# Kernel tuning notes

Measured on AMD Instinct MI355X. Metric: run time of the kernel, lower is better.

## Reference

```python
import jax, jax.numpy as jnp
import numpy as np

NEG_INF = -9e15  # matches torch's -9000000000000000.0 mask value
ALPHA = 0.2      # LeakyReLU negative slope


def setup_inputs() -> dict:
    key = jax.random.key(0)
    k1, k2, k3, k4 = jax.random.split(key, 4)
    B, N, Fin, Fout = 8, 2048, 256, 256
    h = jax.random.normal(k1, (B, N, Fin), dtype=jnp.float32)
    adj = jax.random.randint(k2, (B, N, N), 0, 2, dtype=jnp.int32)
    # xavier_uniform with gain=1.414
    limW = 1.414 * np.sqrt(6.0 / (Fin + Fout))
    W = jax.random.uniform(k3, (Fin, Fout), minval=-limW, maxval=limW, dtype=jnp.float32)
    lima = 1.414 * np.sqrt(6.0 / (2 * Fout + 1))
    a = jax.random.uniform(k4, (2 * Fout, 1), minval=-lima, maxval=lima, dtype=jnp.float32)
    return {"h": h, "adj": adj, "W": W, "a": a}


def reference(h, adj, W, a):
    # h: (B, N, Fin), adj: (B, N, N), W: (Fin, Fout), a: (2*Fout, 1)
    Fout = W.shape[1]
    Wh = jnp.einsum('bni,io->bno', h, W)                 # (B, N, Fout)
    # e[b,i,j] = leakyrelu(Wh[b,i] @ a1 + Wh[b,j] @ a2) -- equivalent to the
    # original concat([Wh_i, Wh_j]) @ a without the O(N^2 * 2F) intermediate.
    e1 = Wh @ a[:Fout, 0]                                # (B, N)
    e2 = Wh @ a[Fout:, 0]                                # (B, N)
    e = jax.nn.leaky_relu(e1[:, :, None] + e2[:, None, :], negative_slope=ALPHA)
    masked = jnp.where(adj > 0, e, NEG_INF)
    attention = jax.nn.softmax(masked, axis=-1)          # (B, N, N)
    # dropout omitted (deterministic eval-mode reference)
    h_prime = jnp.einsum('bij,bjo->bio', attention, Wh)  # (B, N, Fout)
    return jax.nn.elu(h_prime), attention
```

## Files before the change

kernel.cpp:

```cpp
#include <hip/hip_runtime.h>
#include <hip/hip_bf16.h>
#include <stdint.h>

#define NEG_INF -9.0e15f
#define LRELU_ALPHA 0.2f
#define LOG2E 1.442695040888963f

using bf16x8  = __attribute__((ext_vector_type(8))) short;
using f32x4   = __attribute__((ext_vector_type(4))) float;
using short4v = __attribute__((ext_vector_type(4))) short;
using int4v   = __attribute__((ext_vector_type(4))) int;
using float4v = __attribute__((ext_vector_type(4))) float;
using uint2v  = __attribute__((ext_vector_type(2))) unsigned;
using uint4v  = __attribute__((ext_vector_type(4))) unsigned;

static __device__ __forceinline__ short f2bf(float f) {
  unsigned u = __builtin_bit_cast(unsigned, f);
  u = u + 0x7FFFu + ((u >> 16) & 1u);
  return (short)(u >> 16);
}
static __device__ __forceinline__ unsigned cvtpk_bf16(float lo, float hi) {
  unsigned r;
  asm volatile("v_cvt_pk_bf16_f32 %0, %1, %2" : "=v"(r) : "v"(lo), "v"(hi));
  return r;
}
static __device__ __forceinline__ void gload16(const void* g, void* l) {
  __builtin_amdgcn_global_load_lds((const __attribute__((address_space(1))) void*)g,
                                   (__attribute__((address_space(3))) void*)l, 16, 0, 0);
}

__global__ __launch_bounds__(256) void prep_kernel(
    const float* __restrict__ W, const float* __restrict__ a,
    short* __restrict__ W_t, float* __restrict__ aW1, float* __restrict__ aW2)
{
  const int bid = blockIdx.x;
  const int tid = threadIdx.x;
  if (bid < 16) {
    __shared__ float t[64][65];
    const int m0 = (bid & 3) * 64, n0 = (bid >> 2) * 64;
    const int rr = tid >> 3, cc = (tid & 7) * 8;
#pragma unroll
    for (int p = 0; p < 2; ++p) {
      int row = rr + p * 32;
      const float* sp = W + (m0 + row) * 256 + n0 + cc;
      float4v v0 = *(const float4v*)sp;
      float4v v1 = *(const float4v*)(sp + 4);
#pragma unroll
      for (int j = 0; j < 4; ++j) { t[row][cc + j] = v0[j]; t[row][cc + 4 + j] = v1[j]; }
    }
    __syncthreads();
#pragma unroll
    for (int p = 0; p < 2; ++p) {
      int orow = rr + p * 32;
      short vv[8] __attribute__((aligned(16)));
#pragma unroll
      for (int j = 0; j < 8; ++j) vv[j] = f2bf(t[cc + j][orow]);
      short* dp = W_t + (n0 + orow) * 256 + m0 + cc;
      *(int4v*)dp = *(const int4v*)vv;
    }
  } else {
    const int r8 = tid >> 3, o4 = (tid & 7) * 4;
    float s1[8] = {}, s2[8] = {};
#pragma unroll
    for (int rp = 0; rp < 8; ++rp) {
      int row = r8 + rp * 32;
#pragma unroll
      for (int k = 0; k < 8; ++k) {
        int o = o4 + k * 32;
        float4v wv = *(const float4v*)(W + row * 256 + o);
        float4v a1 = *(const float4v*)(a + o);
        float4v a2 = *(const float4v*)(a + 256 + o);
#pragma unroll
        for (int e = 0; e < 4; ++e) { s1[rp] += wv[e] * a1[e]; s2[rp] += wv[e] * a2[e]; }
      }
    }
#pragma unroll
    for (int rp = 0; rp < 8; ++rp) {
#pragma unroll
      for (int off = 4; off > 0; off >>= 1) {
        s1[rp] += __shfl_xor(s1[rp], off, 64);
        s2[rp] += __shfl_xor(s2[rp], off, 64);
      }
      if ((tid & 7) == 0) { aW1[r8 + rp * 32] = s1[rp]; aW2[r8 + rp * 32] = s2[rp]; }
    }
  }
}

__global__ __launch_bounds__(256) void gemm_h_kernel(
    const float* __restrict__ A, const short* __restrict__ Bt,
    short* __restrict__ Wht, const float* __restrict__ aW1,
    const float* __restrict__ aW2, float* __restrict__ e1, float* __restrict__ e2)
{
  __shared__ short As[128 * 32];
  __shared__ short Bs[128 * 32];
  __shared__ short T[128][136];
  const int m0 = blockIdx.x * 128, n0 = blockIdx.y * 128;
  const int tid = threadIdx.x;
  const int w = tid >> 6, lane = tid & 63;
  const int wr = w >> 1, wc = w & 1;
  const int g = lane >> 4, lr = lane & 15;
  const bool doE = (blockIdx.y == 0);

  f32x4 acc[4][4] = {};
  float s1q[2] = {0.f, 0.f}, s2q[2] = {0.f, 0.f};

  for (int k0 = 0; k0 < 256; k0 += 32) {
    __syncthreads();
#pragma unroll
    for (int q = 0; q < 2; ++q) {
      int c = q * 256 + tid;
      int row = c >> 2, kq = (c & 3) << 3;
      const float* ap = A + (long long)(m0 + row) * 256 + k0 + kq;
      float4v u0 = *(const float4v*)ap;
      float4v u1 = *(const float4v*)(ap + 4);
      if (doE) {
        float4v w1a = *(const float4v*)(aW1 + k0 + kq);
        float4v w1b = *(const float4v*)(aW1 + k0 + kq + 4);
        float4v w2a = *(const float4v*)(aW2 + k0 + kq);
        float4v w2b = *(const float4v*)(aW2 + k0 + kq + 4);
#pragma unroll
        for (int e = 0; e < 4; ++e) {
          s1q[q] += u0[e] * w1a[e] + u1[e] * w1b[e];
          s2q[q] += u0[e] * w2a[e] + u1[e] * w2b[e];
        }
      }
      uint4v uv;
      uv[0] = cvtpk_bf16(u0[0], u0[1]);
      uv[1] = cvtpk_bf16(u0[2], u0[3]);
      uv[2] = cvtpk_bf16(u1[0], u1[1]);
      uv[3] = cvtpk_bf16(u1[2], u1[3]);
      *(bf16x8*)(As + c * 8) = __builtin_bit_cast(bf16x8, uv);
    }
#pragma unroll
    for (int q = 0; q < 2; ++q) {
      int p = w * 2 + q;
      int c = p * 64 + lane;
      int row = c >> 2, kq = (c & 3) << 3;
      gload16(Bt + (long long)(n0 + row) * 256 + k0 + kq, Bs + p * 512);
    }
    __syncthreads();

    bf16x8 af[4], bfr[4];
#pragma unroll
    for (int i = 0; i < 4; ++i) {
      af[i]  = *(const bf16x8*)(As + (wr * 64 + i * 16 + lr) * 32 + 8 * g);
      bfr[i] = *(const bf16x8*)(Bs + (wc * 64 + i * 16 + lr) * 32 + 8 * g);
    }
#pragma unroll
    for (int i = 0; i < 4; ++i)
#pragma unroll
      for (int j = 0; j < 4; ++j)
        acc[i][j] = __builtin_amdgcn_mfma_f32_16x16x32_bf16(af[i], bfr[j], acc[i][j], 0, 0, 0);
  }

  if (doE) {
#pragma unroll
    for (int q = 0; q < 2; ++q) {
      float a1 = s1q[q], a2 = s2q[q];
      a1 += __shfl_xor(a1, 1, 64); a1 += __shfl_xor(a1, 2, 64);
      a2 += __shfl_xor(a2, 1, 64); a2 += __shfl_xor(a2, 2, 64);
      if ((tid & 3) == 0) {
        int row = m0 + q * 64 + (tid >> 2);
        e1[row] = a1; e2[row] = a2;
      }
    }
  }

  __syncthreads();
#pragma unroll
  for (int i = 0; i < 4; ++i) {
    int row_base = wr * 64 + i * 16 + 4 * g;
#pragma unroll
    for (int j = 0; j < 4; ++j) {
      int col = wc * 64 + j * 16 + lr;
#pragma unroll
      for (int r = 0; r < 4; ++r)
        T[col][row_base + r] = f2bf(acc[i][j][r]);
    }
  }
  __syncthreads();
  const int b = m0 >> 11, mloc = m0 & 2047;
  short* wb = Wht + (long long)b * 524288 + mloc;
#pragma unroll
  for (int p = 0; p < 8; ++p) {
    int c = (tid >> 4) + p * 16;
    int off = (tid & 15) * 8;
    bf16x8 v = *(const bf16x8*)(&T[c][off]);
    *(bf16x8*)(wb + (long long)(n0 + c) * 2048 + off) = v;
  }
}

__global__ __launch_bounds__(256) void pack_kernel(
    const int* __restrict__ adj, const float* __restrict__ e1,
    const float* __restrict__ e2, float* __restrict__ attn)
{
  const int i = blockIdx.x;
  const int b = blockIdx.y;
  const long long row = (long long)b * 2048 + i;
  const int tid = threadIdx.x;
  const int wid = tid >> 6, lane = tid & 63;
  const int j0 = tid * 8;

  const int*   arow = adj + row * 2048 + j0;
  const float  ei   = e1[row];
  const float* e2b  = e2 + b * 2048 + j0;

  int4v   a0 = *(const int4v*)(arow);
  int4v   a1 = *(const int4v*)(arow + 4);
  float4v f0 = *(const float4v*)(e2b);
  float4v f1 = *(const float4v*)(e2b + 4);

  float s[8];
#pragma unroll
  for (int k = 0; k < 8; ++k) {
    float x = ei + (k < 4 ? f0[k] : f1[k - 4]);
    float v = fmaxf(x, LRELU_ALPHA * x);
    int  ad = (k < 4 ? a0[k] : a1[k - 4]);
    s[k] = (ad > 0) ? v : NEG_INF;
  }
  float m = s[0];
#pragma unroll
  for (int k = 1; k < 8; ++k) m = fmaxf(m, s[k]);
#pragma unroll
  for (int off = 32; off > 0; off >>= 1) m = fmaxf(m, __shfl_xor(m, off, 64));

  __shared__ float wmax[4], wsum[4];
  if (lane == 0) wmax[wid] = m;
  __syncthreads();
  const float M = fmaxf(fmaxf(wmax[0], wmax[1]), fmaxf(wmax[2], wmax[3]));

  float p[8]; float t = 0.f;
#pragma unroll
  for (int k = 0; k < 8; ++k) { p[k] = __expf(s[k] - M); t += p[k]; }
#pragma unroll
  for (int off = 32; off > 0; off >>= 1) t += __shfl_xor(t, off, 64);
  if (lane == 0) wsum[wid] = t;
  __syncthreads();
  const float S = wsum[0] + wsum[1] + wsum[2] + wsum[3];
  const float r = 1.0f / S;

  uint4v uv;
  uv[0] = cvtpk_bf16(p[0] * r, p[1] * r);
  uv[1] = cvtpk_bf16(p[2] * r, p[3] * r);
  uv[2] = cvtpk_bf16(p[4] * r, p[5] * r);
  uv[3] = cvtpk_bf16(p[6] * r, p[7] * r);
  short* op = (short*)(attn + row * 2048 + 1024) + j0;
  *(uint4v*)op = uv;
}

__global__ __launch_bounds__(256, 4) void pv_kernel(
    const short* __restrict__ Bt, float* __restrict__ attnw, float* __restrict__ C)
{
  __shared__ short As0[32 * 32],  As1[32 * 32];
  __shared__ short Bs0[256 * 32], Bs1[256 * 32];
  const int bid = blockIdx.x;
  const int bz  = bid & 7;
  const int M0  = (bid >> 3) << 5;
  const int tid = threadIdx.x;
  const int w = tid >> 6, lane = tid & 63;
  const int g = lane >> 4, lr = lane & 15;

  Bt    += (long long)bz * 524288;
  attnw += (long long)bz * 4194304;
  C     += (long long)bz * 524288;

  const int pr = tid >> 3, k4 = (tid & 7) << 2;
  const int kc = k4 >> 3;
  const int as_off = pr * 32 + ((kc ^ ((pr >> 1) & 3)) << 3) + (k4 & 7);
  float* arow = attnw + (long long)(M0 + pr) * 2048;

  const int bcol_off = lane >> 2;
  const int bchunk   = (lane & 3) ^ ((lane >> 3) & 3);

  const int a_s  = w * 64 + lane;
  const int a_r  = a_s >> 2, a_cs = a_s & 3;
  const int a_dc = a_cs ^ ((a_r >> 1) & 3);
  const short* aP = (const short*)(attnw + (long long)(M0 + a_r) * 2048 + 1024) + a_dc * 8;

  f32x4 acc[2][4] = {};

  auto STAGE = [&](short* BsD, short* AsD, int k0) {
#pragma unroll
    for (int q = 0; q < 4; ++q) {
      int pp = w * 4 + q;
      int col = pp * 16 + bcol_off;
      gload16(Bt + (long long)col * 2048 + k0 + bchunk * 8, BsD + pp * 512);
    }
    if (w < 2) gload16(aP + k0, AsD + w * 512);
  };

  auto COMPUTE = [&](const short* BsD, const short* AsD, int k0) {
    uint2v pw = *(const uint2v*)(AsD + as_off);
    float4v o;
    o[0] = __builtin_bit_cast(float, pw[0] << 16);
    o[1] = __builtin_bit_cast(float, pw[0] & 0xFFFF0000u);
    o[2] = __builtin_bit_cast(float, pw[1] << 16);
    o[3] = __builtin_bit_cast(float, pw[1] & 0xFFFF0000u);
    *(float4v*)(arow + k0 + k4) = o;

    bf16x8 af[2], bfr[4];
#pragma unroll
    for (int i = 0; i < 2; ++i) {
      int row = i * 16 + lr;
      af[i] = *(const bf16x8*)(AsD + row * 32 + ((g ^ ((row >> 1) & 3)) << 3));
    }
#pragma unroll
    for (int j = 0; j < 4; ++j) {
      int col = w * 64 + j * 16 + lr;
      bfr[j] = *(const bf16x8*)(BsD + col * 32 + ((g ^ ((col >> 1) & 3)) << 3));
    }
#pragma unroll
    for (int i = 0; i < 2; ++i)
#pragma unroll
      for (int j = 0; j < 4; ++j)
        acc[i][j] = __builtin_amdgcn_mfma_f32_16x16x32_bf16(af[i], bfr[j], acc[i][j], 0, 0, 0);
  };

  STAGE(Bs0, As0, 0);
  __syncthreads();
  for (int t = 0; t < 64; t += 2) {
    STAGE(Bs1, As1, (t + 1) * 32);
    COMPUTE(Bs0, As0, t * 32);
    __syncthreads();
    if (t + 2 < 64) STAGE(Bs0, As0, (t + 2) * 32);
    COMPUTE(Bs1, As1, (t + 1) * 32);
    __syncthreads();
  }

#pragma unroll
  for (int i = 0; i < 2; ++i) {
    int row_base = M0 + i * 16 + 4 * g;
#pragma unroll
    for (int j = 0; j < 4; ++j) {
      int col = w * 64 + j * 16 + lr;
#pragma unroll
      for (int r = 0; r < 4; ++r) {
        float v = acc[i][j][r];
        v = (v > 0.f) ? v : (__expf(v) - 1.f);
        C[(long long)(row_base + r) * 256 + col] = v;
      }
    }
  }
}

extern "C" void kernel_launch(void* const* d_in, const int* in_sizes, int n_in,
                              void* d_out, int out_size, void* d_ws, size_t ws_size,
                              hipStream_t stream)
{
  const float* h   = (const float*)d_in[0];
  const int*   adj = (const int*)d_in[1];
  const float* W   = (const float*)d_in[2];
  const float* a   = (const float*)d_in[3];

  float* hp_out   = (float*)d_out;
  float* attn_out = hp_out + 4194304LL;

  short* W_t  = (short*)d_ws;
  short* Wh_t = W_t + 65536;
  float* e1   = (float*)(Wh_t + 4194304);
  float* e2   = e1 + 16384;
  float* aW1  = e2 + 16384;
  float* aW2  = aW1 + 256;

  prep_kernel<<<17, 256, 0, stream>>>(W, a, W_t, aW1, aW2);
  gemm_h_kernel<<<dim3(128, 2), 256, 0, stream>>>(h, W_t, Wh_t, aW1, aW2, e1, e2);
  pack_kernel<<<dim3(2048, 8), 256, 0, stream>>>(adj, e1, e2, attn_out);
  pv_kernel<<<512, 256, 0, stream>>>(Wh_t, attn_out, hp_out);
}
```

Before: 121.9 us.

## Write fp32 attention in softmax kernel and convert to bf16 inside PV

The softmax kernel now writes the final fp32 attention directly, where it used to store a packed bf16 copy in the second half of each output row. The PV kernel stages fp32 attention tiles into LDS with an XOR swizzle and converts them to bf16 just before the MFMA. This removes the per-tile fp32 writeback that PV previously did from its bf16 staging buffer. Total attention traffic is roughly unchanged; the trade is that PV becomes read-only on attention but loads twice the bytes per tile, and its LDS tiles double in size, so launch bounds drop from 4 to 3 blocks. LeakyReLU is also rewritten as a select.

```diff
diff --git a/kernel.cpp b/kernel.cpp
--- a/kernel.cpp
+++ b/kernel.cpp
@@ -190,7 +190,7 @@
   }
 }
 
-__global__ __launch_bounds__(256) void pack_kernel(
+__global__ __launch_bounds__(256) void attn_softmax_kernel(
     const int* __restrict__ adj, const float* __restrict__ e1,
     const float* __restrict__ e2, float* __restrict__ attn)
 {
@@ -214,7 +214,7 @@
 #pragma unroll
   for (int k = 0; k < 8; ++k) {
     float x = ei + (k < 4 ? f0[k] : f1[k - 4]);
-    float v = fmaxf(x, LRELU_ALPHA * x);
+    float v = x > 0.f ? x : LRELU_ALPHA * x;
     int  ad = (k < 4 ? a0[k] : a1[k - 4]);
     s[k] = (ad > 0) ? v : NEG_INF;
   }
@@ -239,19 +239,18 @@
   const float S = wsum[0] + wsum[1] + wsum[2] + wsum[3];
   const float r = 1.0f / S;
 
-  uint4v uv;
-  uv[0] = cvtpk_bf16(p[0] * r, p[1] * r);
-  uv[1] = cvtpk_bf16(p[2] * r, p[3] * r);
-  uv[2] = cvtpk_bf16(p[4] * r, p[5] * r);
-  uv[3] = cvtpk_bf16(p[6] * r, p[7] * r);
-  short* op = (short*)(attn + row * 2048 + 1024) + j0;
-  *(uint4v*)op = uv;
-}
-
-__global__ __launch_bounds__(256, 4) void pv_kernel(
-    const short* __restrict__ Bt, float* __restrict__ attnw, float* __restrict__ C)
-{
-  __shared__ short As0[32 * 32],  As1[32 * 32];
+  float4v o0, o1;
+#pragma unroll
+  for (int k = 0; k < 4; ++k) { o0[k] = p[k] * r; o1[k] = p[k + 4] * r; }
+  float* op = attn + row * 2048 + j0;
+  *(float4v*)op       = o0;
+  *(float4v*)(op + 4) = o1;
+}
+
+__global__ __launch_bounds__(256, 3) void pv_kernel(
+    const float* __restrict__ attn, const short* __restrict__ Bt, float* __restrict__ C)
+{
+  __shared__ float As0[32 * 32], As1[32 * 32];
   __shared__ short Bs0[256 * 32], Bs1[256 * 32];
   const int bid = blockIdx.x;
   const int bz  = bid & 7;
@@ -260,49 +259,44 @@
   const int w = tid >> 6, lane = tid & 63;
   const int g = lane >> 4, lr = lane & 15;
 
-  Bt    += (long long)bz * 524288;
-  attnw += (long long)bz * 4194304;
-  C     += (long long)bz * 524288;
-
-  const int pr = tid >> 3, k4 = (tid & 7) << 2;
-  const int kc = k4 >> 3;
-  const int as_off = pr * 32 + ((kc ^ ((pr >> 1) & 3)) << 3) + (k4 & 7);
-  float* arow = attnw + (long long)(M0 + pr) * 2048;
+  attn += (long long)bz * 4194304;
+  Bt   += (long long)bz * 524288;
+  C    += (long long)bz * 524288;
+
+  const int a_s  = w * 64 + lane;
+  const int a_r  = a_s >> 3, a_cs = a_s & 7;
+  const int a_dc = a_cs ^ (a_r & 7);
+  const float* aSrc = attn + (long long)(M0 + a_r) * 2048 + a_dc * 4;
 
   const int bcol_off = lane >> 2;
   const int bchunk   = (lane & 3) ^ ((lane >> 3) & 3);
 
-  const int a_s  = w * 64 + lane;
-  const int a_r  = a_s >> 2, a_cs = a_s & 3;
-  const int a_dc = a_cs ^ ((a_r >> 1) & 3);
-  const short* aP = (const short*)(attnw + (long long)(M0 + a_r) * 2048 + 1024) + a_dc * 8;
-
   f32x4 acc[2][4] = {};
 
-  auto STAGE = [&](short* BsD, short* AsD, int k0) {
+  auto STAGE = [&](short* BsD, float* AsD, int k0) {
 #pragma unroll
     for (int q = 0; q < 4; ++q) {
       int pp = w * 4 + q;
       int col = pp * 16 + bcol_off;
       gload16(Bt + (long long)col * 2048 + k0 + bchunk * 8, BsD + pp * 512);
     }
-    if (w < 2) gload16(aP + k0, AsD + w * 512);
+    gload16(aSrc + k0, (char*)AsD + w * 1024);
   };
 
-  auto COMPUTE = [&](const short* BsD, const short* AsD, int k0) {
-    uint2v pw = *(const uint2v*)(AsD + as_off);
-    float4v o;
-    o[0] = __builtin_bit_cast(float, pw[0] << 16);
-    o[1] = __builtin_bit_cast(float, pw[0] & 0xFFFF0000u);
-    o[2] = __builtin_bit_cast(float, pw[1] << 16);
-    o[3] = __builtin_bit_cast(float, pw[1] & 0xFFFF0000u);
-    *(float4v*)(arow + k0 + k4) = o;
-
+  auto COMPUTE = [&](const short* BsD, const float* AsD) {
     bf16x8 af[2], bfr[4];
 #pragma unroll
     for (int i = 0; i < 2; ++i) {
       int row = i * 16 + lr;
-      af[i] = *(const bf16x8*)(AsD + row * 32 + ((g ^ ((row >> 1) & 3)) << 3));
+      const float* ar = AsD + row * 32;
+      float4v lo = *(const float4v*)(ar + (((2 * g)     ^ (row & 7)) << 2));
+      float4v hi = *(const float4v*)(ar + (((2 * g + 1) ^ (row & 7)) << 2));
+      uint4v uv;
+      uv[0] = cvtpk_bf16(lo[0], lo[1]);
+      uv[1] = cvtpk_bf16(lo[2], lo[3]);
+      uv[2] = cvtpk_bf16(hi[0], hi[1]);
+      uv[3] = cvtpk_bf16(hi[2], hi[3]);
+      af[i] = __builtin_bit_cast(bf16x8, uv);
     }
 #pragma unroll
     for (int j = 0; j < 4; ++j) {
@@ -320,10 +314,10 @@
   __syncthreads();
   for (int t = 0; t < 64; t += 2) {
     STAGE(Bs1, As1, (t + 1) * 32);
-    COMPUTE(Bs0, As0, t * 32);
+    COMPUTE(Bs0, As0);
     __syncthreads();
     if (t + 2 < 64) STAGE(Bs0, As0, (t + 2) * 32);
-    COMPUTE(Bs1, As1, (t + 1) * 32);
+    COMPUTE(Bs1, As1);
     __syncthreads();
   }
 
@@ -364,6 +358,6 @@
 
   prep_kernel<<<17, 256, 0, stream>>>(W, a, W_t, aW1, aW2);
   gemm_h_kernel<<<dim3(128, 2), 256, 0, stream>>>(h, W_t, Wh_t, aW1, aW2, e1, e2);
-  pack_kernel<<<dim3(2048, 8), 256, 0, stream>>>(adj, e1, e2, attn_out);
-  pv_kernel<<<512, 256, 0, stream>>>(Wh_t, attn_out, hp_out);
-}
+  attn_softmax_kernel<<<dim3(2048, 8), 256, 0, stream>>>(adj, e1, e2, attn_out);
+  pv_kernel<<<512, 256, 0, stream>>>(attn_out, Wh_t, hp_out);
+}
```

Result: no change. 121.6 us (-0.3%).
